# Kernel tuning notes

Measured on AMD Instinct MI355X. Metric: run time of the kernel, lower is better.

## Reference

```python
import jax, jax.numpy as jnp
import numpy as np


def _patch_desc(x, patch_size):
    # x: (n, c, h, w). Replicate-pad by patch_size//2 and gather all
    # patch_size*patch_size shifted views -> (n, c*p*p, h*w) descriptors.
    n, c, h, w = x.shape
    step = patch_size // 2
    y = jnp.pad(x, ((0, 0), (0, 0), (step, step), (step, step)), mode='edge')
    feats = [y[:, :, i:i + h, j:j + w]
             for i in range(patch_size) for j in range(patch_size)]
    d = jnp.stack(feats, axis=2)            # (n, c, p*p, h, w)
    return d.reshape(n, c * patch_size * patch_size, h * w)


def setup_inputs() -> dict:
    key = jax.random.key(0)
    k1, k2 = jax.random.split(key)
    n, c, h, w = 4, 16, 64, 64
    s = jax.random.normal(k1, (n, c, h, w), dtype=jnp.float32)
    t = jax.random.normal(k2, (n, c, h, w), dtype=jnp.float32)
    return {"s": s, "t": t, "patch_size": 3}


def reference(s, t, patch_size):
    n, c, h, w = s.shape
    q = _patch_desc(s, patch_size)          # (n, d, hw) source queries
    p = _patch_desc(t, patch_size)          # (n, d, hw) target points
    # Squared-L2 nearest neighbor per source patch (exact version of FLANN kNN)
    qn = jnp.sum(q * q, axis=1)             # (n, hw)
    pn = jnp.sum(p * p, axis=1)             # (n, hw)
    cross = jnp.einsum('ndi,ndj->nij', q, p)  # (n, hw_q, hw_t)
    d2 = qn[:, :, None] - 2.0 * cross + pn[:, None, :]
    idx = jnp.argmin(d2, axis=2)            # (n, hw) flat target index
    nnd = jnp.min(d2, axis=2)               # (n, hw) squared distance
    idy = idx // w
    idx_x = idx % w
    nnf = jnp.stack([idy.reshape(n, h, w), idx_x.reshape(n, h, w)], axis=1)
    nnd = nnd.reshape(n, 1, h, w)
    return nnf.astype(jnp.int32), nnd
```

## Files before the change

kernel.cpp:

```cpp
#include <hip/hip_runtime.h>


#define N_  4
#define C_  16
#define H_  64
#define W_  64
#define HW_ 4096
#define K_  160
#define SPLITS_M 4
#define KKSTRIDE 520

#define SPLITS_V 4
#define TILES_PER_SPLIT_V 4

typedef _Float16 f16;
typedef _Float16 f16x8 __attribute__((ext_vector_type(8)));
typedef float    f32x4 __attribute__((ext_vector_type(4)));

__device__ __forceinline__ int iclamp(int v, int lo, int hi) {
    return v < lo ? lo : (v > hi ? hi : v);
}

__device__ __forceinline__ void async_ld16(const void* g, void* l) {
    __builtin_amdgcn_global_load_lds(
        (const __attribute__((address_space(1))) unsigned int*)g,
        (__attribute__((address_space(3))) unsigned int*)l, 16, 0, 0);
}

__global__ __launch_bounds__(256)
void build_desc_norms_kernel(const float* __restrict__ s,
                             const float* __restrict__ t,
                             f16* __restrict__ Qh, f16* __restrict__ Ql,
                             f16* __restrict__ Ph, f16* __restrict__ Pl,
                             float* __restrict__ pn,
                             float* __restrict__ qn) {
    const int y0  = blockIdx.x * 4;
    const int n   = blockIdx.y;
    const int src = blockIdx.z;
    const float* img = (src ? s : t) + n * (C_ * HW_);
    f16* Dh = src ? Qh : Ph;
    f16* Dl = src ? Ql : Pl;
    float* nrm = src ? qn : pn;

    __shared__ float imgS[C_][8][W_];
    const int tid = threadIdx.x;
    #pragma unroll
    for (int k = 0; k < 32; ++k) {
        const int idx = tid + k * 256;
        const int x = idx & 63, r = (idx >> 6) & 7, c = idx >> 9;
        const int gy = iclamp(y0 + r - 1, 0, H_ - 1);
        imgS[c][r][x] = img[c * HW_ + gy * W_ + x];
    }
    __syncthreads();

    const int ly = tid >> 6, x = tid & 63;
    const int pix = (y0 + ly) * W_ + x;
    float nacc = 0.f;
    #pragma unroll
    for (int kk = 0; kk < 18; ++kk) {
        const int d  = kk >> 1;
        const int c0 = (kk & 1) * 8;
        const int dy = d / 3, dx = d - dy * 3;
        const int rr = ly + dy;
        const int xs = iclamp(x + dx - 1, 0, W_ - 1);
        f16x8 hv, lv;
        #pragma unroll
        for (int cc = 0; cc < 8; ++cc) {
            const float v = imgS[c0 + cc][rr][xs];
            const f16 h = (f16)v;
            hv[cc] = h;
            lv[cc] = (f16)(v - (float)h);
            nacc += v * v;
        }
        const size_t off = ((size_t)(n * 20 + kk) * HW_ + pix) * 8;
        *(f16x8*)&Dh[off] = hv;
        *(f16x8*)&Dl[off] = lv;
    }
    f16x8 z;
    #pragma unroll
    for (int cc = 0; cc < 8; ++cc) z[cc] = (f16)0.f;
    #pragma unroll
    for (int kk = 18; kk < 20; ++kk) {
        const size_t off = ((size_t)(n * 20 + kk) * HW_ + pix) * 8;
        *(f16x8*)&Dh[off] = z;
        *(f16x8*)&Dl[off] = z;
    }
    nrm[n * HW_ + pix] = nacc;
}

__global__ __launch_bounds__(256)
void mfma_nn_kernel(const f16* __restrict__ Qh, const f16* __restrict__ Ql,
                    const f16* __restrict__ Ph, const f16* __restrict__ Pl,
                    const float* __restrict__ pn_g,
                    unsigned long long* __restrict__ partial) {
    const int bid   = blockIdx.x;
    const int split = bid & 3;
    const int n     = (bid >> 2) & 3;
    const int iblk  = bid >> 4;
    const int tid  = threadIdx.x;
    const int wave = tid >> 6, lane = tid & 63;
    const int m = lane & 15, quad = lane >> 4;
    const int irow0 = iblk * 128 + wave * 32;

    __shared__ f16 B[2][20 * KKSTRIDE];

    f16x8 Ah[2][5], Al[2][5];
    #pragma unroll
    for (int is = 0; is < 2; ++is)
        #pragma unroll
        for (int kc = 0; kc < 5; ++kc) {
            const size_t off = ((size_t)(n * 20 + kc * 4 + quad) * HW_ +
                                irow0 + is * 16 + m) * 8;
            Ah[is][kc] = *(const f16x8*)(Qh + off);
            Al[is][kc] = *(const f16x8*)(Ql + off);
        }

    float    bd[2][4];
    unsigned bj[2][4];
    #pragma unroll
    for (int is = 0; is < 2; ++is)
        #pragma unroll
        for (int rg = 0; rg < 4; ++rg) { bd[is][rg] = 3.0e38f; bj[is][rg] = 0u; }

    const int jsplit0 = split * 1024;
    const int skk  = wave * 5;
    const int sarr = lane >> 5;
    const int srow = lane & 31;
    const f16* sbase = sarr ? Pl : Ph;

    #define STAGE(BUFI, J0)                                                   \
        {   _Pragma("unroll")                                                 \
            for (int u = 0; u < 5; ++u) {                                     \
                const int kk = skk + u;                                       \
                const f16* g = sbase +                                        \
                    ((size_t)(n * 20 + kk) * HW_ + (J0) + srow) * 8;          \
                async_ld16(g, (void*)&B[BUFI][kk * KKSTRIDE + lane * 8]);     \
            }                                                                 \
        }

    STAGE(0, jsplit0)
    asm volatile("s_waitcnt vmcnt(0)" ::: "memory");
    __syncthreads();

    for (int jt = 0; jt < 32; ++jt) {
        const int j0  = jsplit0 + jt * 32;
        const int cur = jt & 1;
        if (jt + 1 < 32) STAGE(cur ^ 1, j0 + 32)
        const f16* buf = &B[cur][0];

        #pragma unroll
        for (int js = 0; js < 2; ++js) {
            f32x4 Cf[2];
            Cf[0] = (f32x4){0.f, 0.f, 0.f, 0.f};
            Cf[1] = (f32x4){0.f, 0.f, 0.f, 0.f};
            #pragma unroll
            for (int kc = 0; kc < 5; ++kc) {
                const int kb = (kc * 4 + quad) * KKSTRIDE + (js * 16 + m) * 8;
                const f16x8 bh = *(const f16x8*)&buf[kb];
                const f16x8 bl = *(const f16x8*)&buf[kb + 256];
                #pragma unroll
                for (int is = 0; is < 2; ++is) {
                    Cf[is] = __builtin_amdgcn_mfma_f32_16x16x32_f16(
                        Ah[is][kc], bh, Cf[is], 0, 0, 0);
                    Cf[is] = __builtin_amdgcn_mfma_f32_16x16x32_f16(
                        Al[is][kc], bh, Cf[is], 0, 0, 0);
                    Cf[is] = __builtin_amdgcn_mfma_f32_16x16x32_f16(
                        Ah[is][kc], bl, Cf[is], 0, 0, 0);
                }
            }
            const int jcol = j0 + js * 16 + m;
            const float pnv = pn_g[n * HW_ + jcol];
            #pragma unroll
            for (int is = 0; is < 2; ++is)
                #pragma unroll
                for (int rg = 0; rg < 4; ++rg) {
                    const float d = fmaf(Cf[is][rg], -2.f, pnv);
                    if (d < bd[is][rg]) {
                        bd[is][rg] = d;
                        bj[is][rg] = (unsigned)jcol;
                    }
                }
        }
        asm volatile("s_waitcnt vmcnt(0)" ::: "memory");
        __syncthreads();
    }
    #undef STAGE

    #pragma unroll
    for (int is = 0; is < 2; ++is)
        #pragma unroll
        for (int rg = 0; rg < 4; ++rg) {
            float    d = bd[is][rg];
            unsigned j = bj[is][rg];
            #pragma unroll
            for (int off = 1; off < 16; off <<= 1) {
                const float    od = __shfl_xor(d, off, 64);
                const unsigned oj = __shfl_xor(j, off, 64);
                const bool take = (od < d) || (od == d && oj < j);
                d = take ? od : d;
                j = take ? oj : j;
            }
            if (m == 0) {
                const int i = irow0 + is * 16 + quad * 4 + rg;
                partial[(size_t)(split * N_ + n) * HW_ + i] =
                    ((unsigned long long)j << 32) |
                    (unsigned long long)__float_as_uint(d);
            }
        }
}

__global__ __launch_bounds__(256)
void finalize_mfma_kernel(const unsigned long long* __restrict__ partial,
                          const float* __restrict__ qn_g,
                          float* __restrict__ out) {
    const int id  = blockIdx.x * 256 + threadIdx.x;
    const int n   = id >> 12;
    const int pix = id & 4095;
    float    bd = 3.0e38f;
    unsigned bj = 0u;
    #pragma unroll
    for (int sp = 0; sp < SPLITS_M; ++sp) {
        const unsigned long long v = partial[(size_t)(sp * N_ + n) * HW_ + pix];
        const float    d = __uint_as_float((unsigned)(v & 0xffffffffull));
        const unsigned j = (unsigned)(v >> 32);
        const bool take = (d < bd) || (d == bd && j < bj);
        bd = take ? d : bd;
        bj = take ? j : bj;
    }
    out[n * 2 * HW_ + pix]            = (float)(bj >> 6);
    out[n * 2 * HW_ + HW_ + pix]      = (float)(bj & 63);
    out[N_ * 2 * HW_ + n * HW_ + pix] = bd + qn_g[n * HW_ + pix];
}

__global__ __launch_bounds__(256)
void prep_norms_kernel(const float* __restrict__ s,
                       const float* __restrict__ t,
                       float* __restrict__ pn,
                       float* __restrict__ qn) {
    const int gid   = blockIdx.x * 256 + threadIdx.x;
    const int which = gid >> 14;
    const int id    = gid & 16383;
    const int n     = id >> 12;
    const int pix   = id & 4095;
    const int y = pix >> 6, x = pix & 63;
    const float* base = (which ? s : t) + n * (C_ * HW_);
    float acc = 0.f;
    for (int c = 0; c < C_; ++c) {
        const float* bc = base + c * HW_;
        #pragma unroll
        for (int dy = 0; dy < 3; ++dy) {
            const float* br = bc + iclamp(y + dy - 1, 0, H_ - 1) * W_;
            #pragma unroll
            for (int dx = 0; dx < 3; ++dx) {
                float v = br[iclamp(x + dx - 1, 0, W_ - 1)];
                acc += v * v;
            }
        }
    }
    (which ? qn : pn)[id] = acc;
}

__global__ __launch_bounds__(256)
void patchmatch_main_kernel(const float* __restrict__ s,
                            const float* __restrict__ t,
                            const float* __restrict__ pn_g,
                            const float* __restrict__ qn_g,
                            unsigned long long* __restrict__ partial) {
    const int yq    = blockIdx.x;
    const int n     = blockIdx.y;
    const int split = blockIdx.z;
    const int tid  = threadIdx.x;
    const int tx   = tid & 15;
    const int ty   = tid >> 4;
    const int i0   = ty * 4;
    const int jrow = tx >> 2;
    const int jx0  = (tx & 3) * 16;

    __shared__ float qS[C_][3][68];
    __shared__ float tS[C_][6][68];
    __shared__ float qnS[W_];

    const float* sb = s + n * (C_ * HW_);
    const float* tb = t + n * (C_ * HW_);

    #pragma unroll
    for (int k = 0; k < 3; ++k) {
        const int id = tid + k * 256;
        const int sg = id & 15;
        const int c  = (id >> 4) & 15;
        const int r  = id >> 8;
        const int gr = iclamp(yq + r - 1, 0, H_ - 1);
        const float4 v = *(const float4*)&sb[c * HW_ + gr * W_ + sg * 4];
        float* dst = &qS[c][r][1 + sg * 4];
        dst[0] = v.x; dst[1] = v.y; dst[2] = v.z; dst[3] = v.w;
    }
    if (tid < 48) {
        const int c  = tid & 15;
        const int r  = tid >> 4;
        const int gr = iclamp(yq + r - 1, 0, H_ - 1);
        qS[c][r][0]  = sb[c * HW_ + gr * W_];
        qS[c][r][65] = sb[c * HW_ + gr * W_ + 63];
    }
    if (tid < W_) qnS[tid] = qn_g[n * HW_ + yq * W_ + tid];

    unsigned long long best[4] = {~0ull, ~0ull, ~0ull, ~0ull};

    for (int ytl = 0; ytl < TILES_PER_SPLIT_V; ++ytl) {
        const int yt = split * TILES_PER_SPLIT_V + ytl;
        __syncthreads();
        #pragma unroll
        for (int k = 0; k < 6; ++k) {
            const int id = tid + k * 256;
            const int sg = id & 15;
            const int c  = (id >> 4) & 15;
            const int r  = id >> 8;
            const int gr = iclamp(4 * yt + r - 1, 0, H_ - 1);
            const float4 v = *(const float4*)&tb[c * HW_ + gr * W_ + sg * 4];
            float* dst = &tS[c][r][1 + sg * 4];
            dst[0] = v.x; dst[1] = v.y; dst[2] = v.z; dst[3] = v.w;
        }
        if (tid < 96) {
            const int c  = tid & 15;
            const int r  = tid >> 4;
            const int gr = iclamp(4 * yt + r - 1, 0, H_ - 1);
            tS[c][r][0]  = tb[c * HW_ + gr * W_];
            tS[c][r][65] = tb[c * HW_ + gr * W_ + 63];
        }
        __syncthreads();

        float acc[4][16];
        #pragma unroll
        for (int a = 0; a < 4; ++a)
            #pragma unroll
            for (int b = 0; b < 16; ++b) acc[a][b] = 0.f;

        for (int c = 0; c < C_; ++c) {
            #pragma unroll
            for (int dy = 0; dy < 3; ++dy) {
                float qv[6], tv[18];
                *(float4*)&qv[0] = *(const float4*)&qS[c][dy][i0];
                *(float2*)&qv[4] = *(const float2*)&qS[c][dy][i0 + 4];
                const float* trow = &tS[c][jrow + dy][jx0];
                *(float4*)&tv[0]  = *(const float4*)&trow[0];
                *(float4*)&tv[4]  = *(const float4*)&trow[4];
                *(float4*)&tv[8]  = *(const float4*)&trow[8];
                *(float4*)&tv[12] = *(const float4*)&trow[12];
                *(float2*)&tv[16] = *(const float2*)&trow[16];
                #pragma unroll
                for (int dx = 0; dx < 3; ++dx)
                    #pragma unroll
                    for (int a = 0; a < 4; ++a)
                        #pragma unroll
                        for (int b = 0; b < 16; ++b)
                            acc[a][b] += qv[a + dx] * tv[b + dx];
            }
        }

        const int jbase = yt * 256 + jrow * W_ + jx0;
        float pnv[16];
        const float* png = &pn_g[n * HW_ + jbase];
        *(float4*)&pnv[0]  = *(const float4*)&png[0];
        *(float4*)&pnv[4]  = *(const float4*)&png[4];
        *(float4*)&pnv[8]  = *(const float4*)&png[8];
        *(float4*)&pnv[12] = *(const float4*)&png[12];
        #pragma unroll
        for (int a = 0; a < 4; ++a) {
            const float qn = qnS[i0 + a];
            #pragma unroll
            for (int b = 0; b < 16; ++b) {
                const float d2 = qn + pnv[b] - 2.f * acc[a][b];
                unsigned long long cand =
                    ((unsigned long long)__float_as_uint(d2) << 32) |
                    (unsigned)(jbase + b);
                best[a] = cand < best[a] ? cand : best[a];
            }
        }
    }

    #pragma unroll
    for (int a = 0; a < 4; ++a) {
        unsigned long long v = best[a];
        #pragma unroll
        for (int mm = 8; mm >= 1; mm >>= 1) {
            unsigned long long o = __shfl_xor(v, mm, 64);
            v = o < v ? o : v;
        }
        best[a] = v;
    }
    if (tx == 0) {
        #pragma unroll
        for (int a = 0; a < 4; ++a)
            partial[((split * N_ + n) * HW_) + yq * W_ + i0 + a] = best[a];
    }
}

__global__ __launch_bounds__(256)
void finalize_kernel(const unsigned long long* __restrict__ partial,
                     float* __restrict__ out) {
    const int id  = blockIdx.x * 256 + threadIdx.x;
    const int n   = id >> 12;
    const int pix = id & 4095;
    unsigned long long best = ~0ull;
    #pragma unroll
    for (int sp = 0; sp < SPLITS_V; ++sp) {
        unsigned long long v = partial[(sp * N_ + n) * HW_ + pix];
        best = v < best ? v : best;
    }
    const unsigned j = (unsigned)(best & 0xffffffffu);
    const float d2 = __uint_as_float((unsigned)(best >> 32));
    out[n * 2 * HW_ + pix]            = (float)(j >> 6);
    out[n * 2 * HW_ + HW_ + pix]      = (float)(j & 63);
    out[N_ * 2 * HW_ + n * HW_ + pix] = d2;
}

__global__ __launch_bounds__(256)
void patchmatch_mono_kernel(const float* __restrict__ s,
                            const float* __restrict__ t,
                            float* __restrict__ out) {
    const int yq  = blockIdx.x;
    const int n   = blockIdx.y;
    const int tid = threadIdx.x;
    const int tx  = tid & 15;
    const int ty  = tid >> 4;
    const int i0  = ty * 4;
    const int jrow = tx >> 3;
    const int jx0  = (tx & 7) * 8;

    __shared__ float qS[C_][3][68];
    __shared__ float tS[C_][4][68];
    __shared__ float pnS[HW_];
    __shared__ float qnS[W_];

    const float* sb = s + n * (C_ * HW_);
    const float* tb = t + n * (C_ * HW_);

    for (int jj = tid; jj < HW_; jj += 256) {
        const int y = jj >> 6, x = jj & 63;
        float acc = 0.f;
        for (int c = 0; c < C_; ++c) {
            const float* tc = tb + c * HW_;
            #pragma unroll
            for (int dy = 0; dy < 3; ++dy) {
                const float* tr = tc + iclamp(y + dy - 1, 0, H_ - 1) * W_;
                #pragma unroll
                for (int dx = 0; dx < 3; ++dx) {
                    float v = tr[iclamp(x + dx - 1, 0, W_ - 1)];
                    acc += v * v;
                }
            }
        }
        pnS[jj] = acc;
    }
    for (int idx = tid; idx < C_ * 3 * 66; idx += 256) {
        const int c   = idx / (3 * 66);
        const int rem = idx - c * (3 * 66);
        const int rr  = rem / 66;
        const int xi  = rem - rr * 66;
        qS[c][rr][xi] = sb[c * HW_ + iclamp(yq + rr - 1, 0, H_ - 1) * W_ +
                           iclamp(xi - 1, 0, W_ - 1)];
    }
    __syncthreads();
    if (tid < W_) {
        float acc = 0.f;
        for (int c = 0; c < C_; ++c)
            #pragma unroll
            for (int dy = 0; dy < 3; ++dy)
                #pragma unroll
                for (int dx = 0; dx < 3; ++dx) {
                    float v = qS[c][dy][tid + dx];
                    acc += v * v;
                }
        qnS[tid] = acc;
    }

    unsigned long long best[4] = {~0ull, ~0ull, ~0ull, ~0ull};
    for (int yt = 0; yt < 32; ++yt) {
        __syncthreads();
        for (int idx = tid; idx < C_ * 4 * 66; idx += 256) {
            const int c   = idx / (4 * 66);
            const int rem = idx - c * (4 * 66);
            const int rr  = rem / 66;
            const int xi  = rem - rr * 66;
            tS[c][rr][xi] = tb[c * HW_ + iclamp(2 * yt + rr - 1, 0, H_ - 1) * W_ +
                               iclamp(xi - 1, 0, W_ - 1)];
        }
        __syncthreads();

        float acc[4][8];
        #pragma unroll
        for (int a = 0; a < 4; ++a)
            #pragma unroll
            for (int b = 0; b < 8; ++b) acc[a][b] = 0.f;

        for (int c = 0; c < C_; ++c) {
            #pragma unroll
            for (int dy = 0; dy < 3; ++dy) {
                float qv[8], tv[12];
                *(float4*)&qv[0] = *(const float4*)&qS[c][dy][i0];
                *(float4*)&qv[4] = *(const float4*)&qS[c][dy][i0 + 4];
                const float* trow = &tS[c][jrow + dy][jx0];
                *(float4*)&tv[0] = *(const float4*)&trow[0];
                *(float4*)&tv[4] = *(const float4*)&trow[4];
                *(float4*)&tv[8] = *(const float4*)&trow[8];
                #pragma unroll
                for (int dx = 0; dx < 3; ++dx)
                    #pragma unroll
                    for (int a = 0; a < 4; ++a)
                        #pragma unroll
                        for (int b = 0; b < 8; ++b)
                            acc[a][b] += qv[a + dx] * tv[b + dx];
            }
        }
        const int rbase = (2 * yt + jrow) * W_ + jx0;
        #pragma unroll
        for (int a = 0; a < 4; ++a) {
            const float qn = qnS[i0 + a];
            #pragma unroll
            for (int b = 0; b < 8; ++b) {
                const int j = rbase + b;
                const float d2 = qn + pnS[j] - 2.f * acc[a][b];
                unsigned long long cand =
                    ((unsigned long long)__float_as_uint(d2) << 32) | (unsigned)j;
                best[a] = cand < best[a] ? cand : best[a];
            }
        }
    }
    #pragma unroll
    for (int a = 0; a < 4; ++a) {
        unsigned long long v = best[a];
        #pragma unroll
        for (int mm = 8; mm >= 1; mm >>= 1) {
            unsigned long long o = __shfl_xor(v, mm, 64);
            v = o < v ? o : v;
        }
        best[a] = v;
    }
    if (tx == 0) {
        #pragma unroll
        for (int a = 0; a < 4; ++a) {
            const int x = i0 + a;
            const unsigned j = (unsigned)(best[a] & 0xffffffffu);
            const float d2 = __uint_as_float((unsigned)(best[a] >> 32));
            const int pix = yq * W_ + x;
            out[n * 2 * HW_ + pix]            = (float)(j >> 6);
            out[n * 2 * HW_ + HW_ + pix]      = (float)(j & 63);
            out[N_ * 2 * HW_ + n * HW_ + pix] = d2;
        }
    }
}

extern "C" void kernel_launch(void* const* d_in, const int* in_sizes, int n_in,
                              void* d_out, int out_size, void* d_ws, size_t ws_size,
                              hipStream_t stream) {
    const float* s = (const float*)d_in[0];
    const float* t = (const float*)d_in[1];
    float* out = (float*)d_out;

    const size_t norm_b  = (size_t)N_ * HW_ * 4;
    const size_t part_b  = (size_t)SPLITS_M * N_ * HW_ * 8;
    const size_t desc_b  = (size_t)N_ * HW_ * K_ * 2;
    const size_t need_m  = 2 * norm_b + part_b + 4 * desc_b;

    if (ws_size >= need_m) {
        char* w = (char*)d_ws;
        float* pn = (float*)w;                       w += norm_b;
        float* qn = (float*)w;                       w += norm_b;
        unsigned long long* partial = (unsigned long long*)w; w += part_b;
        f16* Qh = (f16*)w;  w += desc_b;
        f16* Ql = (f16*)w;  w += desc_b;
        f16* Ph = (f16*)w;  w += desc_b;
        f16* Pl = (f16*)w;

        build_desc_norms_kernel<<<dim3(16, N_, 2), 256, 0, stream>>>(
            s, t, Qh, Ql, Ph, Pl, pn, qn);
        mfma_nn_kernel<<<512, 256, 0, stream>>>(Qh, Ql, Ph, Pl, pn, partial);
        finalize_mfma_kernel<<<64, 256, 0, stream>>>(partial, qn, out);
        return;
    }

    const size_t need_v = 2 * norm_b + (size_t)SPLITS_V * N_ * HW_ * 8;
    if (ws_size >= need_v) {
        float* pn = (float*)d_ws;
        float* qn = pn + N_ * HW_;
        unsigned long long* partial =
            (unsigned long long*)((char*)d_ws + 2 * norm_b);
        prep_norms_kernel<<<128, 256, 0, stream>>>(s, t, pn, qn);
        dim3 grid(H_, N_, SPLITS_V);
        patchmatch_main_kernel<<<grid, 256, 0, stream>>>(s, t, pn, qn, partial);
        finalize_kernel<<<64, 256, 0, stream>>>(partial, out);
        return;
    }

    dim3 grid(H_, N_);
    patchmatch_mono_kernel<<<grid, 256, 0, stream>>>(s, t, out);
}
```

Measured before the change: 132.4 us.

## Triple-buffer MFMA B tiles, cache target norms in LDS, re-split descriptor build

The NN kernel moves from double to triple buffering of the async LDS tile loads. It uses partial vmcnt waits with raw barriers so the next tile's loads overlap compute, and pads the LDS row stride. Target norms are preloaded into shared memory instead of read from global memory per column. The descriptor build kernel now runs one row per block across 4x more blocks, splitting the k-chunks across waves and reducing norms through LDS. This adds LDS usage and relies on the hand-written vmcnt counts being correct.

```diff
diff --git a/kernel.cpp b/kernel.cpp
--- a/kernel.cpp
+++ b/kernel.cpp
@@ -8,7 +8,7 @@
 #define HW_ 4096
 #define K_  160
 #define SPLITS_M 4
-#define KKSTRIDE 520
+#define KKSTRIDE 528
 
 #define SPLITS_V 4
 #define TILES_PER_SPLIT_V 4
@@ -34,7 +34,7 @@
                              f16* __restrict__ Ph, f16* __restrict__ Pl,
                              float* __restrict__ pn,
                              float* __restrict__ qn) {
-    const int y0  = blockIdx.x * 4;
+    const int y0  = blockIdx.x;
     const int n   = blockIdx.y;
     const int src = blockIdx.z;
     const float* img = (src ? s : t) + n * (C_ * HW_);
@@ -42,50 +42,51 @@
     f16* Dl = src ? Ql : Pl;
     float* nrm = src ? qn : pn;
 
-    __shared__ float imgS[C_][8][W_];
+    __shared__ float imgS[3][C_][W_];
+    __shared__ float nS[4][W_];
     const int tid = threadIdx.x;
     #pragma unroll
-    for (int k = 0; k < 32; ++k) {
+    for (int k = 0; k < 12; ++k) {
         const int idx = tid + k * 256;
-        const int x = idx & 63, r = (idx >> 6) & 7, c = idx >> 9;
+        const int x = idx & 63, c = (idx >> 6) & 15, r = idx >> 10;
         const int gy = iclamp(y0 + r - 1, 0, H_ - 1);
-        imgS[c][r][x] = img[c * HW_ + gy * W_ + x];
+        imgS[r][c][x] = img[c * HW_ + gy * W_ + x];
     }
     __syncthreads();
 
-    const int ly = tid >> 6, x = tid & 63;
-    const int pix = (y0 + ly) * W_ + x;
+    const int q = tid >> 6, x = tid & 63;
+    const int pix = y0 * W_ + x;
     float nacc = 0.f;
     #pragma unroll
-    for (int kk = 0; kk < 18; ++kk) {
-        const int d  = kk >> 1;
-        const int c0 = (kk & 1) * 8;
-        const int dy = d / 3, dx = d - dy * 3;
-        const int rr = ly + dy;
-        const int xs = iclamp(x + dx - 1, 0, W_ - 1);
+    for (int u = 0; u < 5; ++u) {
+        const int kk = q * 5 + u;
         f16x8 hv, lv;
-        #pragma unroll
-        for (int cc = 0; cc < 8; ++cc) {
-            const float v = imgS[c0 + cc][rr][xs];
-            const f16 h = (f16)v;
-            hv[cc] = h;
-            lv[cc] = (f16)(v - (float)h);
-            nacc += v * v;
+        if (kk < 18) {
+            const int d  = kk >> 1;
+            const int c0 = (kk & 1) * 8;
+            const int dy = (d * 11) >> 5;
+            const int dx = d - dy * 3;
+            const int xs = iclamp(x + dx - 1, 0, W_ - 1);
+            #pragma unroll
+            for (int cc = 0; cc < 8; ++cc) {
+                const float v = imgS[dy][c0 + cc][xs];
+                const f16 h = (f16)v;
+                hv[cc] = h;
+                lv[cc] = (f16)(v - (float)h);
+                nacc += v * v;
+            }
+        } else {
+            #pragma unroll
+            for (int cc = 0; cc < 8; ++cc) { hv[cc] = (f16)0.f; lv[cc] = (f16)0.f; }
         }
         const size_t off = ((size_t)(n * 20 + kk) * HW_ + pix) * 8;
         *(f16x8*)&Dh[off] = hv;
         *(f16x8*)&Dl[off] = lv;
     }
-    f16x8 z;
-    #pragma unroll
-    for (int cc = 0; cc < 8; ++cc) z[cc] = (f16)0.f;
-    #pragma unroll
-    for (int kk = 18; kk < 20; ++kk) {
-        const size_t off = ((size_t)(n * 20 + kk) * HW_ + pix) * 8;
-        *(f16x8*)&Dh[off] = z;
-        *(f16x8*)&Dl[off] = z;
-    }
-    nrm[n * HW_ + pix] = nacc;
+    nS[q][x] = nacc;
+    __syncthreads();
+    if (tid < W_)
+        nrm[n * HW_ + pix] = nS[0][tid] + nS[1][tid] + nS[2][tid] + nS[3][tid];
 }
 
 __global__ __launch_bounds__(256)
@@ -102,7 +103,10 @@
     const int m = lane & 15, quad = lane >> 4;
     const int irow0 = iblk * 128 + wave * 32;
 
-    __shared__ f16 B[2][20 * KKSTRIDE];
+    __shared__ f16 B0[20 * KKSTRIDE];
+    __shared__ f16 B1[20 * KKSTRIDE];
+    __shared__ f16 B2[20 * KKSTRIDE];
+    __shared__ float pnS[1024];
 
     f16x8 Ah[2][5], Al[2][5];
     #pragma unroll
@@ -115,6 +119,11 @@
             Al[is][kc] = *(const f16x8*)(Ql + off);
         }
 
+    const int jsplit0 = split * 1024;
+    #pragma unroll
+    for (int k = 0; k < 4; ++k)
+        pnS[tid + k * 256] = pn_g[n * HW_ + jsplit0 + tid + k * 256];
+
     float    bd[2][4];
     unsigned bj[2][4];
     #pragma unroll
@@ -122,76 +131,92 @@
         #pragma unroll
         for (int rg = 0; rg < 4; ++rg) { bd[is][rg] = 3.0e38f; bj[is][rg] = 0u; }
 
-    const int jsplit0 = split * 1024;
     const int skk  = wave * 5;
     const int sarr = lane >> 5;
     const int srow = lane & 31;
     const f16* sbase = sarr ? Pl : Ph;
 
-    #define STAGE(BUFI, J0)                                                   \
+    #define STAGE(BUF, T)                                                     \
         {   _Pragma("unroll")                                                 \
             for (int u = 0; u < 5; ++u) {                                     \
                 const int kk = skk + u;                                       \
-                const f16* g = sbase +                                        \
-                    ((size_t)(n * 20 + kk) * HW_ + (J0) + srow) * 8;          \
-                async_ld16(g, (void*)&B[BUFI][kk * KKSTRIDE + lane * 8]);     \
+                const f16* g = sbase + ((size_t)(n * 20 + kk) * HW_ +         \
+                                        jsplit0 + (T) * 32 + srow) * 8;       \
+                async_ld16(g, (void*)&BUF[kk * KKSTRIDE + lane * 8]);         \
             }                                                                 \
         }
 
-    STAGE(0, jsplit0)
+    #define COMPUTE(BUF, T)                                                   \
+        {   _Pragma("unroll")                                                 \
+            for (int js = 0; js < 2; ++js) {                                  \
+                f32x4 Cf[2];                                                  \
+                Cf[0] = (f32x4){0.f, 0.f, 0.f, 0.f};                          \
+                Cf[1] = (f32x4){0.f, 0.f, 0.f, 0.f};                          \
+                _Pragma("unroll")                                             \
+                for (int kc = 0; kc < 5; ++kc) {                              \
+                    const int kb = (kc * 4 + quad) * KKSTRIDE +               \
+                                   (js * 16 + m) * 8;                         \
+                    const f16x8 bh = *(const f16x8*)&BUF[kb];                 \
+                    const f16x8 bl = *(const f16x8*)&BUF[kb + 256];           \
+                    _Pragma("unroll")                                         \
+                    for (int is = 0; is < 2; ++is) {                          \
+                        Cf[is] = __builtin_amdgcn_mfma_f32_16x16x32_f16(      \
+                            Ah[is][kc], bh, Cf[is], 0, 0, 0);                 \
+                        Cf[is] = __builtin_amdgcn_mfma_f32_16x16x32_f16(      \
+                            Al[is][kc], bh, Cf[is], 0, 0, 0);                 \
+                        Cf[is] = __builtin_amdgcn_mfma_f32_16x16x32_f16(      \
+                            Ah[is][kc], bl, Cf[is], 0, 0, 0);                 \
+                    }                                                         \
+                }                                                             \
+                const int jloc = (T) * 32 + js * 16 + m;                      \
+                const float pnv = pnS[jloc];                                  \
+                _Pragma("unroll")                                             \
+                for (int is = 0; is < 2; ++is)                                \
+                    _Pragma("unroll")                                         \
+                    for (int rg = 0; rg < 4; ++rg) {                          \
+                        const float d = fmaf(Cf[is][rg], -2.f, pnv);          \
+                        if (d < bd[is][rg]) {                                 \
+                            bd[is][rg] = d;                                   \
+                            bj[is][rg] = (unsigned)jloc;                      \
+                        }                                                     \
+                    }                                                         \
+            }                                                                 \
+        }
+
+    STAGE(B0, 0)
+    STAGE(B1, 1)
+    __syncthreads();
+
+    for (int g = 0; g < 10; ++g) {
+        const int t = g * 3;
+        asm volatile("s_waitcnt vmcnt(5)" ::: "memory");
+        asm volatile("s_barrier" ::: "memory");
+        STAGE(B2, t + 2)
+        COMPUTE(B0, t)
+        asm volatile("s_waitcnt vmcnt(5)" ::: "memory");
+        asm volatile("s_barrier" ::: "memory");
+        STAGE(B0, t + 3)
+        COMPUTE(B1, t + 1)
+        asm volatile("s_waitcnt vmcnt(5)" ::: "memory");
+        asm volatile("s_barrier" ::: "memory");
+        STAGE(B1, t + 4)
+        COMPUTE(B2, t + 2)
+    }
+    asm volatile("s_waitcnt vmcnt(5)" ::: "memory");
+    asm volatile("s_barrier" ::: "memory");
+    COMPUTE(B0, 30)
     asm volatile("s_waitcnt vmcnt(0)" ::: "memory");
-    __syncthreads();
-
-    for (int jt = 0; jt < 32; ++jt) {
-        const int j0  = jsplit0 + jt * 32;
-        const int cur = jt & 1;
-        if (jt + 1 < 32) STAGE(cur ^ 1, j0 + 32)
-        const f16* buf = &B[cur][0];
-
-        #pragma unroll
-        for (int js = 0; js < 2; ++js) {
-            f32x4 Cf[2];
-            Cf[0] = (f32x4){0.f, 0.f, 0.f, 0.f};
-            Cf[1] = (f32x4){0.f, 0.f, 0.f, 0.f};
-            #pragma unroll
-            for (int kc = 0; kc < 5; ++kc) {
-                const int kb = (kc * 4 + quad) * KKSTRIDE + (js * 16 + m) * 8;
-                const f16x8 bh = *(const f16x8*)&buf[kb];
-                const f16x8 bl = *(const f16x8*)&buf[kb + 256];
-                #pragma unroll
-                for (int is = 0; is < 2; ++is) {
-                    Cf[is] = __builtin_amdgcn_mfma_f32_16x16x32_f16(
-                        Ah[is][kc], bh, Cf[is], 0, 0, 0);
-                    Cf[is] = __builtin_amdgcn_mfma_f32_16x16x32_f16(
-                        Al[is][kc], bh, Cf[is], 0, 0, 0);
-                    Cf[is] = __builtin_amdgcn_mfma_f32_16x16x32_f16(
-                        Ah[is][kc], bl, Cf[is], 0, 0, 0);
-                }
-            }
-            const int jcol = j0 + js * 16 + m;
-            const float pnv = pn_g[n * HW_ + jcol];
-            #pragma unroll
-            for (int is = 0; is < 2; ++is)
-                #pragma unroll
-                for (int rg = 0; rg < 4; ++rg) {
-                    const float d = fmaf(Cf[is][rg], -2.f, pnv);
-                    if (d < bd[is][rg]) {
-                        bd[is][rg] = d;
-                        bj[is][rg] = (unsigned)jcol;
-                    }
-                }
-        }
-        asm volatile("s_waitcnt vmcnt(0)" ::: "memory");
-        __syncthreads();
-    }
+    asm volatile("s_barrier" ::: "memory");
+    COMPUTE(B1, 31)
     #undef STAGE
+    #undef COMPUTE
 
     #pragma unroll
     for (int is = 0; is < 2; ++is)
         #pragma unroll
         for (int rg = 0; rg < 4; ++rg) {
             float    d = bd[is][rg];
-            unsigned j = bj[is][rg];
+            unsigned j = (unsigned)jsplit0 + bj[is][rg];
             #pragma unroll
             for (int off = 1; off < 16; off <<= 1) {
                 const float    od = __shfl_xor(d, off, 64);
@@ -571,7 +596,7 @@
         f16* Ph = (f16*)w;  w += desc_b;
         f16* Pl = (f16*)w;
 
-        build_desc_norms_kernel<<<dim3(16, N_, 2), 256, 0, stream>>>(
+        build_desc_norms_kernel<<<dim3(64, N_, 2), 256, 0, stream>>>(
             s, t, Qh, Ql, Ph, Pl, pn, qn);
         mfma_nn_kernel<<<512, 256, 0, stream>>>(Qh, Ql, Ph, Pl, pn, partial);
         finalize_mfma_kernel<<<64, 256, 0, stream>>>(partial, qn, out);
```

Result: faster. 124.8 us (-5.7%).
